# Optimization experiments

Hardware: AMD Instinct MI355X
Metric: run time of the kernel (lower is better)

Reference implementation:

```python
import jax, jax.numpy as jnp
import numpy as np

N, C, F = 64, 128, 2048


def setup_inputs() -> dict:
    key = jax.random.key(0)
    kx, ka = jax.random.split(key)
    X = jax.random.normal(kx, (N, C, F), dtype=jnp.float32)
    # Glorot-uniform init for A [C, C, F]: fan_in = C*F, fan_out = C*F
    limit = np.sqrt(6.0 / (C * F + C * F)).astype(np.float32)
    A = jax.random.uniform(ka, (C, C, F), dtype=jnp.float32, minval=-limit, maxval=limit)
    return {"X": X, "A": A}


def reference(X, A):
    # scores: reduce feature dim F -> [N, C, M]
    c = jnp.einsum('ncf,cmf->ncm', X, A)
    W = jax.nn.softmax(c, axis=-1)  # attention over source channels M
    # combine: mix channels of X with attention weights -> [N, C, F]
    return jnp.einsum('nmf,ncm->ncf', X, W)
```

## Files before the change

### kernel.cpp

```cpp
#include <hip/hip_runtime.h>


typedef __attribute__((ext_vector_type(8))) short bf16x8;
typedef __attribute__((ext_vector_type(4))) float f32x4;

#define PART_E (64 * 128 * 128)
#define NP 8

static __device__ __forceinline__ unsigned f2bf_pk(float a, float b) {
    unsigned ua = __float_as_uint(a);
    unsigned ub = __float_as_uint(b);
    ua = (ua + 0x7FFFu + ((ua >> 16) & 1u)) >> 16;
    ub = (ub + 0x7FFFu + ((ub >> 16) & 1u)) >> 16;
    return ua | (ub << 16);
}
static __device__ __forceinline__ unsigned short f2bf1(float a) {
    unsigned ua = __float_as_uint(a);
    ua = (ua + 0x7FFFu + ((ua >> 16) & 1u)) >> 16;
    return (unsigned short)ua;
}
static __device__ __forceinline__ float bf2f(unsigned s) {
    return __uint_as_float(s << 16);
}
static __device__ __forceinline__ void gl_lds16(const void* g, void* l) {
    __builtin_amdgcn_global_load_lds((const __attribute__((address_space(1))) void*)g,
                                     (__attribute__((address_space(3))) void*)l, 16, 0, 0);
}
static __device__ __forceinline__ bf16x8 cvt8(float4 lo, float4 hi) {
    union { bf16x8 v; unsigned u[4]; } r;
    r.u[0] = f2bf_pk(lo.x, lo.y);
    r.u[1] = f2bf_pk(lo.z, lo.w);
    r.u[2] = f2bf_pk(hi.x, hi.y);
    r.u[3] = f2bf_pk(hi.z, hi.w);
    return r.v;
}

__global__ __launch_bounds__(256, 4) void k_scores(const float* __restrict__ X,
                                                   const float* __restrict__ A,
                                                   unsigned short* __restrict__ part) {
    __shared__ float Xs[64 * 32];
    __shared__ float As[128 * 32];

    const int bx = blockIdx.x;
    const int c = bx >> 3;
    const int p = bx & 7;
    const int t = threadIdx.x;
    const int l = t & 63;
    const int w = t >> 6;
    const int l15 = l & 15;
    const int lg = l >> 4;
    const int wn = (w & 1) * 32;
    const int wm = (w >> 1) * 64;

    const int lr = l >> 3;
    const int lq = (l & 7) ^ lr;

    f32x4 acc[2][4];
#pragma unroll
    for (int i = 0; i < 2; ++i)
#pragma unroll
        for (int j = 0; j < 4; ++j) acc[i][j] = (f32x4)0.0f;

    const int s0 = (lg * 2) ^ (l15 & 7);
    const int s1 = (lg * 2 + 1) ^ (l15 & 7);

    for (int kb = 0; kb < 8; ++kb) {
        const int f = p * 256 + kb * 32 + lq * 4;
#pragma unroll
        for (int ii = 0; ii < 2; ++ii) {
            const int I = 2 * w + ii;
            const int r = I * 8 + lr;
            gl_lds16(X + ((size_t)r * 128 + c) * 2048 + f, &Xs[I * 256]);
        }
#pragma unroll
        for (int ii = 0; ii < 4; ++ii) {
            const int I = 4 * w + ii;
            const int r = I * 8 + lr;
            gl_lds16(A + ((size_t)c * 128 + r) * 2048 + f, &As[I * 256]);
        }
        __syncthreads();

        bf16x8 a[2], b[4];
#pragma unroll
        for (int i = 0; i < 2; ++i) {
            const float4* row = (const float4*)&Xs[(wn + 16 * i + l15) * 32];
            a[i] = cvt8(row[s0], row[s1]);
        }
#pragma unroll
        for (int j = 0; j < 4; ++j) {
            const float4* row = (const float4*)&As[(wm + 16 * j + l15) * 32];
            b[j] = cvt8(row[s0], row[s1]);
        }
#pragma unroll
        for (int i = 0; i < 2; ++i)
#pragma unroll
            for (int j = 0; j < 4; ++j)
                acc[i][j] = __builtin_amdgcn_mfma_f32_16x16x32_bf16(a[i], b[j], acc[i][j], 0, 0, 0);
        __syncthreads();
    }

    unsigned short* op = part + (size_t)p * PART_E;
#pragma unroll
    for (int i = 0; i < 2; ++i) {
        const int nb = wn + 16 * i + lg * 4;
#pragma unroll
        for (int j = 0; j < 4; ++j) {
            const int m = wm + 16 * j + l15;
#pragma unroll
            for (int r = 0; r < 4; ++r)
                op[((size_t)(nb + r) * 128 + c) * 128 + m] = f2bf1(acc[i][j][r]);
        }
    }
}

__global__ __launch_bounds__(256) void k_softmax(const unsigned int* __restrict__ part,
                                                 unsigned int* __restrict__ Wout) {
    const int t = threadIdx.x;
    const int l = t & 63;
    const int row = blockIdx.x * 4 + (t >> 6);

    float v0 = 0.f, v1 = 0.f;
#pragma unroll
    for (int p = 0; p < NP; ++p) {
        unsigned u = part[(size_t)p * (PART_E / 2) + (size_t)row * 64 + l];
        v0 += bf2f(u & 0xFFFFu);
        v1 += bf2f(u >> 16);
    }
    float mx = fmaxf(v0, v1);
#pragma unroll
    for (int d = 1; d < 64; d <<= 1) mx = fmaxf(mx, __shfl_xor(mx, d, 64));
    float e0 = __expf(v0 - mx), e1 = __expf(v1 - mx);
    float sm = e0 + e1;
#pragma unroll
    for (int d = 1; d < 64; d <<= 1) sm += __shfl_xor(sm, d, 64);
    const float inv = 1.0f / sm;
    Wout[(size_t)row * 64 + l] = f2bf_pk(e0 * inv, e1 * inv);
}

__global__ __launch_bounds__(256, 3) void k_combine(const float* __restrict__ X,
                                                    const unsigned short* __restrict__ W,
                                                    float* __restrict__ out) {
    __shared__ unsigned short Wl[128 * 128];
    __shared__ float Xs[32 * 128];

    const int bx = blockIdx.x;
    const int n = bx >> 4;
    const int f0 = (bx & 15) * 128;
    const int t = threadIdx.x;
    const int l = t & 63;
    const int w = t >> 6;
    const int l15 = l & 15;
    const int lg = l >> 4;
    const int wc = (w >> 1) * 64;
    const int wf = (w & 1) * 64;

    {
        const int lr = l >> 4;
        const int sl = l & 15;
#pragma unroll
        for (int ii = 0; ii < 8; ++ii) {
            const int I = 8 * w + ii;
            const int r = I * 4 + lr;
            const int q = (sl & 8) | ((sl ^ r) & 7);
            gl_lds16(W + (size_t)n * 16384 + r * 128 + q * 8, &Wl[I * 512]);
        }
    }

    f32x4 acc[4][4];
#pragma unroll
    for (int i = 0; i < 4; ++i)
#pragma unroll
        for (int j = 0; j < 4; ++j) acc[i][j] = (f32x4)0.0f;

    const int lr2 = l >> 5;
    const int q2 = l & 31;

    for (int m0 = 0; m0 < 128; m0 += 32) {
#pragma unroll
        for (int ii = 0; ii < 4; ++ii) {
            const int I = 4 * w + ii;
            const int r = I * 2 + lr2;
            gl_lds16(X + ((size_t)n * 128 + m0 + r) * 2048 + f0 + q2 * 4, &Xs[I * 256]);
        }
        __syncthreads();

        bf16x8 a[4], b[4];
#pragma unroll
        for (int i = 0; i < 4; ++i) {
            const int cr = wc + 16 * i + l15;
            const int q = (m0 >> 3) + lg;
            const int s = (q & 8) | ((q ^ cr) & 7);
            a[i] = *(const bf16x8*)&Wl[cr * 128 + s * 8];
        }
#pragma unroll
        for (int j = 0; j < 4; ++j) {
            const float* col = &Xs[(lg * 8) * 128 + wf + 16 * j + l15];
            float v[8];
#pragma unroll
            for (int rr = 0; rr < 8; ++rr) v[rr] = col[rr * 128];
            union { bf16x8 bv; unsigned u[4]; } r_;
            r_.u[0] = f2bf_pk(v[0], v[1]);
            r_.u[1] = f2bf_pk(v[2], v[3]);
            r_.u[2] = f2bf_pk(v[4], v[5]);
            r_.u[3] = f2bf_pk(v[6], v[7]);
            b[j] = r_.bv;
        }
#pragma unroll
        for (int i = 0; i < 4; ++i)
#pragma unroll
            for (int j = 0; j < 4; ++j)
                acc[i][j] = __builtin_amdgcn_mfma_f32_16x16x32_bf16(a[i], b[j], acc[i][j], 0, 0, 0);
        __syncthreads();
    }

#pragma unroll
    for (int i = 0; i < 4; ++i) {
        const int c = wc + 16 * i + lg * 4;
#pragma unroll
        for (int j = 0; j < 4; ++j) {
            const int f = f0 + wf + 16 * j + l15;
            float* o = out + ((size_t)n * 128 + c) * 2048 + f;
#pragma unroll
            for (int r = 0; r < 4; ++r) o[(size_t)r * 2048] = acc[i][j][r];
        }
    }
}

extern "C" void kernel_launch(void* const* d_in, const int* in_sizes, int n_in,
                              void* d_out, int out_size, void* d_ws, size_t ws_size,
                              hipStream_t stream) {
    const float* X = (const float*)d_in[0];
    const float* A = (const float*)d_in[1];
    float* out = (float*)d_out;

    unsigned short* part = (unsigned short*)d_ws;
    unsigned short* Wb = part + (size_t)NP * PART_E;

    k_scores<<<dim3(1024), dim3(256), 0, stream>>>(X, A, part);
    k_softmax<<<dim3(2048), dim3(256), 0, stream>>>((const unsigned int*)part, (unsigned int*)Wb);
    k_combine<<<dim3(1024), dim3(256), 0, stream>>>(X, Wb, out);
}
```

Measured before the change: 286.6 us.

## Drop split-K partials and register-prefetch bf16 tiles in scores and combine

The scores kernel no longer splits F across 8 partial blocks. Each of 256 blocks of 512 threads now covers the full F range for one channel and half of M, and writes fp32 scores directly, so the softmax no longer has to sum 8 bf16 partials. Global loads are prefetched into registers, converted to bf16 once and stored into swizzled LDS, which overlaps the next tile's loads with the MFMAs. The combine kernel gets the same register prefetch and larger 512-thread blocks covering 256 features. In exchange, the scores kernel launches far fewer blocks, which may leave the GPU underoccupied, and register pressure rises.

Result: slower. 293.8 us (+2.5%).

```diff
diff --git a/kernel.cpp b/kernel.cpp
--- a/kernel.cpp
+++ b/kernel.cpp
@@ -3,9 +3,6 @@
 
 typedef __attribute__((ext_vector_type(8))) short bf16x8;
 typedef __attribute__((ext_vector_type(4))) float f32x4;
-
-#define PART_E (64 * 128 * 128)
-#define NP 8
 
 static __device__ __forceinline__ unsigned f2bf_pk(float a, float b) {
     unsigned ua = __float_as_uint(a);
@@ -14,122 +11,89 @@
     ub = (ub + 0x7FFFu + ((ub >> 16) & 1u)) >> 16;
     return ua | (ub << 16);
 }
-static __device__ __forceinline__ unsigned short f2bf1(float a) {
-    unsigned ua = __float_as_uint(a);
-    ua = (ua + 0x7FFFu + ((ua >> 16) & 1u)) >> 16;
-    return (unsigned short)ua;
-}
-static __device__ __forceinline__ float bf2f(unsigned s) {
-    return __uint_as_float(s << 16);
-}
-static __device__ __forceinline__ void gl_lds16(const void* g, void* l) {
-    __builtin_amdgcn_global_load_lds((const __attribute__((address_space(1))) void*)g,
-                                     (__attribute__((address_space(3))) void*)l, 16, 0, 0);
-}
-static __device__ __forceinline__ bf16x8 cvt8(float4 lo, float4 hi) {
-    union { bf16x8 v; unsigned u[4]; } r;
-    r.u[0] = f2bf_pk(lo.x, lo.y);
-    r.u[1] = f2bf_pk(lo.z, lo.w);
-    r.u[2] = f2bf_pk(hi.x, hi.y);
-    r.u[3] = f2bf_pk(hi.z, hi.w);
-    return r.v;
-}
-
-__global__ __launch_bounds__(256, 4) void k_scores(const float* __restrict__ X,
+
+__global__ __launch_bounds__(512, 2) void k_scores(const float* __restrict__ X,
                                                    const float* __restrict__ A,
-                                                   unsigned short* __restrict__ part) {
-    __shared__ float Xs[64 * 32];
-    __shared__ float As[128 * 32];
-
-    const int bx = blockIdx.x;
-    const int c = bx >> 3;
-    const int p = bx & 7;
+                                                   float* __restrict__ Sc) {
+    __shared__ short Xb[64 * 256];
+    __shared__ short Ab[64 * 256];
+
+    const int c  = blockIdx.x >> 1;
+    const int mh = blockIdx.x & 1;
     const int t = threadIdx.x;
     const int l = t & 63;
     const int w = t >> 6;
     const int l15 = l & 15;
     const int lg = l >> 4;
-    const int wn = (w & 1) * 32;
-    const int wm = (w >> 1) * 64;
-
-    const int lr = l >> 3;
-    const int lq = (l & 7) ^ lr;
-
-    f32x4 acc[2][4];
-#pragma unroll
-    for (int i = 0; i < 2; ++i)
-#pragma unroll
-        for (int j = 0; j < 4; ++j) acc[i][j] = (f32x4)0.0f;
-
-    const int s0 = (lg * 2) ^ (l15 & 7);
-    const int s1 = (lg * 2 + 1) ^ (l15 & 7);
-
-    for (int kb = 0; kb < 8; ++kb) {
-        const int f = p * 256 + kb * 32 + lq * 4;
-#pragma unroll
-        for (int ii = 0; ii < 2; ++ii) {
-            const int I = 2 * w + ii;
-            const int r = I * 8 + lr;
-            gl_lds16(X + ((size_t)r * 128 + c) * 2048 + f, &Xs[I * 256]);
-        }
-#pragma unroll
-        for (int ii = 0; ii < 4; ++ii) {
-            const int I = 4 * w + ii;
-            const int r = I * 8 + lr;
-            gl_lds16(A + ((size_t)c * 128 + r) * 2048 + f, &As[I * 256]);
+    const int nw = (w & 1) * 32;
+    const int mw = (w >> 1) * 16;
+    const int q = l >> 1;
+    const int h = l & 1;
+
+    const float* Xg = X + ((size_t)(w * 8) * 128 + c) * 2048 + l * 4;
+    const float* Ag = A + ((size_t)c * 128 + mh * 64 + w * 8) * 2048 + l * 4;
+
+    float4 xr[8], ar[8];
+    f32x4 acc[2];
+    acc[0] = (f32x4)0.0f; acc[1] = (f32x4)0.0f;
+
+#pragma unroll
+    for (int r = 0; r < 8; ++r) xr[r] = *(const float4*)(Xg + (size_t)r * (128 * 2048));
+#pragma unroll
+    for (int r = 0; r < 8; ++r) ar[r] = *(const float4*)(Ag + (size_t)r * 2048);
+
+    for (int it = 0; it < 8; ++it) {
+        if (it) __syncthreads();
+#pragma unroll
+        for (int r = 0; r < 8; ++r) {
+            const int row = w * 8 + r;
+            const int s = (q & 24) | ((q ^ (row & 7)) & 7);
+            *(uint2*)&Xb[row * 256 + s * 8 + h * 4] =
+                make_uint2(f2bf_pk(xr[r].x, xr[r].y), f2bf_pk(xr[r].z, xr[r].w));
+            *(uint2*)&Ab[row * 256 + s * 8 + h * 4] =
+                make_uint2(f2bf_pk(ar[r].x, ar[r].y), f2bf_pk(ar[r].z, ar[r].w));
         }
         __syncthreads();
-
-        bf16x8 a[2], b[4];
-#pragma unroll
-        for (int i = 0; i < 2; ++i) {
-            const float4* row = (const float4*)&Xs[(wn + 16 * i + l15) * 32];
-            a[i] = cvt8(row[s0], row[s1]);
-        }
-#pragma unroll
-        for (int j = 0; j < 4; ++j) {
-            const float4* row = (const float4*)&As[(wm + 16 * j + l15) * 32];
-            b[j] = cvt8(row[s0], row[s1]);
-        }
-#pragma unroll
-        for (int i = 0; i < 2; ++i)
-#pragma unroll
-            for (int j = 0; j < 4; ++j)
-                acc[i][j] = __builtin_amdgcn_mfma_f32_16x16x32_bf16(a[i], b[j], acc[i][j], 0, 0, 0);
-        __syncthreads();
-    }
-
-    unsigned short* op = part + (size_t)p * PART_E;
+        if (it < 7) {
+            const int f = (it + 1) * 256;
+#pragma unroll
+            for (int r = 0; r < 8; ++r) xr[r] = *(const float4*)(Xg + (size_t)r * (128 * 2048) + f);
+#pragma unroll
+            for (int r = 0; r < 8; ++r) ar[r] = *(const float4*)(Ag + (size_t)r * 2048 + f);
+        }
+#pragma unroll
+        for (int ks = 0; ks < 8; ++ks) {
+            const int qq = ks * 4 + lg;
+            const int r0 = nw + l15, r1 = nw + 16 + l15, rb = mw + l15;
+            bf16x8 a0 = *(const bf16x8*)&Xb[r0 * 256 + ((qq & 24) | ((qq ^ (r0 & 7)) & 7)) * 8];
+            bf16x8 a1 = *(const bf16x8*)&Xb[r1 * 256 + ((qq & 24) | ((qq ^ (r1 & 7)) & 7)) * 8];
+            bf16x8 b  = *(const bf16x8*)&Ab[rb * 256 + ((qq & 24) | ((qq ^ (rb & 7)) & 7)) * 8];
+            acc[0] = __builtin_amdgcn_mfma_f32_16x16x32_bf16(a0, b, acc[0], 0, 0, 0);
+            acc[1] = __builtin_amdgcn_mfma_f32_16x16x32_bf16(a1, b, acc[1], 0, 0, 0);
+        }
+    }
+
 #pragma unroll
     for (int i = 0; i < 2; ++i) {
-        const int nb = wn + 16 * i + lg * 4;
-#pragma unroll
-        for (int j = 0; j < 4; ++j) {
-            const int m = wm + 16 * j + l15;
-#pragma unroll
-            for (int r = 0; r < 4; ++r)
-                op[((size_t)(nb + r) * 128 + c) * 128 + m] = f2bf1(acc[i][j][r]);
-        }
-    }
-}
-
-__global__ __launch_bounds__(256) void k_softmax(const unsigned int* __restrict__ part,
+        const int n = nw + 16 * i + lg * 4;
+        const int m = mh * 64 + mw + l15;
+        float* o = Sc + ((size_t)n * 128 + c) * 128 + m;
+#pragma unroll
+        for (int r = 0; r < 4; ++r) o[(size_t)r * 16384] = acc[i][r];
+    }
+}
+
+__global__ __launch_bounds__(256) void k_softmax(const float* __restrict__ Sc,
                                                  unsigned int* __restrict__ Wout) {
     const int t = threadIdx.x;
     const int l = t & 63;
     const int row = blockIdx.x * 4 + (t >> 6);
 
-    float v0 = 0.f, v1 = 0.f;
-#pragma unroll
-    for (int p = 0; p < NP; ++p) {
-        unsigned u = part[(size_t)p * (PART_E / 2) + (size_t)row * 64 + l];
-        v0 += bf2f(u & 0xFFFFu);
-        v1 += bf2f(u >> 16);
-    }
-    float mx = fmaxf(v0, v1);
+    float2 v = *(const float2*)(Sc + (size_t)row * 128 + 2 * l);
+    float mx = fmaxf(v.x, v.y);
 #pragma unroll
     for (int d = 1; d < 64; d <<= 1) mx = fmaxf(mx, __shfl_xor(mx, d, 64));
-    float e0 = __expf(v0 - mx), e1 = __expf(v1 - mx);
+    float e0 = __expf(v.x - mx), e1 = __expf(v.y - mx);
     float sm = e0 + e1;
 #pragma unroll
     for (int d = 1; d < 64; d <<= 1) sm += __shfl_xor(sm, d, 64);
@@ -137,34 +101,31 @@
     Wout[(size_t)row * 64 + l] = f2bf_pk(e0 * inv, e1 * inv);
 }
 
-__global__ __launch_bounds__(256, 3) void k_combine(const float* __restrict__ X,
+__global__ __launch_bounds__(512, 4) void k_combine(const float* __restrict__ X,
                                                     const unsigned short* __restrict__ W,
                                                     float* __restrict__ out) {
     __shared__ unsigned short Wl[128 * 128];
-    __shared__ float Xs[32 * 128];
-
-    const int bx = blockIdx.x;
-    const int n = bx >> 4;
-    const int f0 = (bx & 15) * 128;
+    __shared__ float Xs[32 * 256];
+
+    const int n  = blockIdx.x >> 3;
+    const int f0 = (blockIdx.x & 7) * 256;
     const int t = threadIdx.x;
     const int l = t & 63;
     const int w = t >> 6;
     const int l15 = l & 15;
     const int lg = l >> 4;
-    const int wc = (w >> 1) * 64;
-    const int wf = (w & 1) * 64;
-
-    {
-        const int lr = l >> 4;
-        const int sl = l & 15;
-#pragma unroll
-        for (int ii = 0; ii < 8; ++ii) {
-            const int I = 8 * w + ii;
-            const int r = I * 4 + lr;
-            const int q = (sl & 8) | ((sl ^ r) & 7);
-            gl_lds16(W + (size_t)n * 16384 + r * 128 + q * 8, &Wl[I * 512]);
-        }
-    }
+    const int wc = (w & 1) * 64;
+    const int wf = (w >> 1) * 64;
+
+    const uint4* Wg = (const uint4*)(W + (size_t)n * 16384);
+    uint4 wr[4];
+#pragma unroll
+    for (int ro = 0; ro < 4; ++ro) wr[ro] = Wg[ro * 512 + t];
+
+    float4 xr[4];
+#pragma unroll
+    for (int ii = 0; ii < 4; ++ii)
+        xr[ii] = *(const float4*)(X + ((size_t)n * 128 + w * 4 + ii) * 2048 + f0 + l * 4);
 
     f32x4 acc[4][4];
 #pragma unroll
@@ -172,32 +133,43 @@
 #pragma unroll
         for (int j = 0; j < 4; ++j) acc[i][j] = (f32x4)0.0f;
 
-    const int lr2 = l >> 5;
-    const int q2 = l & 31;
-
-    for (int m0 = 0; m0 < 128; m0 += 32) {
-#pragma unroll
-        for (int ii = 0; ii < 4; ++ii) {
-            const int I = 4 * w + ii;
-            const int r = I * 2 + lr2;
-            gl_lds16(X + ((size_t)n * 128 + m0 + r) * 2048 + f0 + q2 * 4, &Xs[I * 256]);
-        }
+    for (int it = 0; it < 4; ++it) {
+        if (it == 0) {
+#pragma unroll
+            for (int ro = 0; ro < 4; ++ro) {
+                const int flat = ro * 512 + t;
+                const int r = flat >> 4;
+                const int qq = flat & 15;
+                const int s = (qq & 8) | ((qq ^ (r & 7)) & 7);
+                *(uint4*)&Wl[r * 128 + s * 8] = wr[ro];
+            }
+        } else {
+            __syncthreads();
+        }
+#pragma unroll
+        for (int ii = 0; ii < 4; ++ii)
+            *(float4*)&Xs[(w * 4 + ii) * 256 + l * 4] = xr[ii];
         __syncthreads();
-
+        if (it < 3) {
+            const int m0 = (it + 1) * 32;
+#pragma unroll
+            for (int ii = 0; ii < 4; ++ii)
+                xr[ii] = *(const float4*)(X + ((size_t)n * 128 + m0 + w * 4 + ii) * 2048 + f0 + l * 4);
+        }
         bf16x8 a[4], b[4];
 #pragma unroll
         for (int i = 0; i < 4; ++i) {
             const int cr = wc + 16 * i + l15;
-            const int q = (m0 >> 3) + lg;
-            const int s = (q & 8) | ((q ^ cr) & 7);
+            const int q2 = it * 4 + lg;
+            const int s = (q2 & 8) | ((q2 ^ (cr & 7)) & 7);
             a[i] = *(const bf16x8*)&Wl[cr * 128 + s * 8];
         }
 #pragma unroll
         for (int j = 0; j < 4; ++j) {
-            const float* col = &Xs[(lg * 8) * 128 + wf + 16 * j + l15];
+            const int col = wf + 16 * j + l15;
             float v[8];
 #pragma unroll
-            for (int rr = 0; rr < 8; ++rr) v[rr] = col[rr * 128];
+            for (int rr = 0; rr < 8; ++rr) v[rr] = Xs[(lg * 8 + rr) * 256 + col];
             union { bf16x8 bv; unsigned u[4]; } r_;
             r_.u[0] = f2bf_pk(v[0], v[1]);
             r_.u[1] = f2bf_pk(v[2], v[3]);
@@ -210,16 +182,15 @@
 #pragma unroll
             for (int j = 0; j < 4; ++j)
                 acc[i][j] = __builtin_amdgcn_mfma_f32_16x16x32_bf16(a[i], b[j], acc[i][j], 0, 0, 0);
-        __syncthreads();
     }
 
 #pragma unroll
     for (int i = 0; i < 4; ++i) {
-        const int c = wc + 16 * i + lg * 4;
+        const int c0 = wc + 16 * i + lg * 4;
 #pragma unroll
         for (int j = 0; j < 4; ++j) {
             const int f = f0 + wf + 16 * j + l15;
-            float* o = out + ((size_t)n * 128 + c) * 2048 + f;
+            float* o = out + ((size_t)n * 128 + c0) * 2048 + f;
 #pragma unroll
             for (int r = 0; r < 4; ++r) o[(size_t)r * 2048] = acc[i][j][r];
         }
@@ -233,10 +204,10 @@
     const float* A = (const float*)d_in[1];
     float* out = (float*)d_out;
 
-    unsigned short* part = (unsigned short*)d_ws;
-    unsigned short* Wb = part + (size_t)NP * PART_E;
-
-    k_scores<<<dim3(1024), dim3(256), 0, stream>>>(X, A, part);
-    k_softmax<<<dim3(2048), dim3(256), 0, stream>>>((const unsigned int*)part, (unsigned int*)Wb);
-    k_combine<<<dim3(1024), dim3(256), 0, stream>>>(X, Wb, out);
-}
+    float* Sc = (float*)d_ws;
+    unsigned short* Wb = (unsigned short*)((char*)d_ws + (size_t)64 * 128 * 128 * 4);
+
+    k_scores<<<dim3(256), dim3(512), 0, stream>>>(X, A, Sc);
+    k_softmax<<<dim3(2048), dim3(256), 0, stream>>>(Sc, (unsigned int*)Wb);
+    k_combine<<<dim3(512), dim3(512), 0, stream>>>(X, Wb, out);
+}
```
